# Kernel optimization log

Hardware: AMD Instinct MI355X
Metric: run time of the kernel (lower is better)

The kernel has to match this reference:

```python
import jax, jax.numpy as jnp
import numpy as np

FEATURE_SIZE = 1_000_000
FIELD_SIZE = 39
EMBED_SIZE = 32
HIDDEN = [400, 400]
BATCH = 16384


def setup_inputs() -> dict:
    key = jax.random.key(0)
    ks = jax.random.split(key, 10)
    p_emb = 1.0 / np.sqrt(FEATURE_SIZE + EMBED_SIZE)
    p_bias = 1.0 / np.sqrt(FEATURE_SIZE + 1)
    d_in = FIELD_SIZE * EMBED_SIZE
    p1 = 1.0 / np.sqrt(d_in + HIDDEN[0])
    p2 = 1.0 / np.sqrt(HIDDEN[0] + HIDDEN[1])
    d_cat = FIELD_SIZE + EMBED_SIZE + HIDDEN[-1]
    pf = 1.0 / np.sqrt(d_cat + 1)
    return {
        "feat_index": jax.random.randint(ks[0], (BATCH, FIELD_SIZE), 0, FEATURE_SIZE),
        "feat_value": jax.random.uniform(ks[1], (BATCH, FIELD_SIZE), dtype=jnp.float32),
        "feature_embedding": jax.random.uniform(ks[2], (FEATURE_SIZE, EMBED_SIZE), jnp.float32, -p_emb, p_emb),
        "feature_bias": jax.random.uniform(ks[3], (FEATURE_SIZE, 1), jnp.float32, -p_bias, p_bias),
        "W1": jax.random.uniform(ks[4], (HIDDEN[0], d_in), jnp.float32, -p1, p1),
        "b1": jnp.zeros((HIDDEN[0],), jnp.float32),
        "W2": jax.random.uniform(ks[5], (HIDDEN[1], HIDDEN[0]), jnp.float32, -p2, p2),
        "b2": jnp.zeros((HIDDEN[1],), jnp.float32),
        "final_W": jax.random.uniform(ks[6], (1, d_cat), jnp.float32, -pf, pf),
        "final_b": jnp.zeros((1,), jnp.float32),
    }


def reference(feat_index, feat_value, feature_embedding, feature_bias,
              W1, b1, W2, b2, final_W, final_b):
    B = feat_index.shape[0]
    fv = feat_value[:, :, None]                          # [B, F, 1]
    emb = feature_embedding[feat_index] * fv             # [B, F, E]

    # first-order FM term: [B, F]
    first_order = jnp.sum(feature_bias[feat_index] * fv, axis=-1)

    # second-order FM term: 0.5 * ((sum e)^2 - sum e^2), [B, E]
    sum_emb = jnp.sum(emb, axis=1)
    second_order = 0.5 * (sum_emb * sum_emb - jnp.sum(emb * emb, axis=1))

    # deep component
    deep_y = emb.reshape(B, FIELD_SIZE * EMBED_SIZE)
    deep_y = jax.nn.relu(deep_y @ W1.T + b1)
    deep_y = jax.nn.relu(deep_y @ W2.T + b2)

    concat_input = jnp.concatenate([first_order, second_order, deep_y], axis=1)
    output = concat_input @ final_W.T + final_b          # [B, 1]
    return (output, first_order, second_order, deep_y)
```

## Files before the change

kernel.cpp:

```cpp
#include <hip/hip_runtime.h>
#include <hip/hip_bf16.h>

#define BATCH 16384
#define FIELD 39
#define EMB 32
#define DIN (FIELD * EMB)
#define HID 400
#define DCAT (FIELD + EMB + HID)

typedef __attribute__((ext_vector_type(8))) short short8;
typedef __attribute__((ext_vector_type(4))) float float4v;

static __device__ __forceinline__ unsigned short f2bf(float f) {
    __hip_bfloat16 h = __float2bfloat16(f);
    return *(unsigned short*)&h;
}

__global__ __launch_bounds__(256) void gather_fm_kernel(
    const int* __restrict__ feat_index,
    const float* __restrict__ feat_value,
    const float* __restrict__ emb_table,
    const float* __restrict__ bias_table,
    unsigned short* __restrict__ emb_ws,
    float* __restrict__ first_order,
    float* __restrict__ second_order)
{
    __shared__ int   s_idx[FIELD];
    __shared__ float s_val[FIELD];
    __shared__ float s_emb[FIELD][EMB];

    const int r = blockIdx.x;
    const int t = threadIdx.x;

    if (t < FIELD) {
        int   idx = feat_index[r * FIELD + t];
        float val = feat_value[r * FIELD + t];
        s_idx[t] = idx;
        s_val[t] = val;
        first_order[r * FIELD + t] = bias_table[idx] * val;
    }
    __syncthreads();

    for (int e = t; e < DIN; e += 256) {
        const int f = e >> 5;
        const int j = e & 31;
        float v = emb_table[(size_t)s_idx[f] * EMB + j] * s_val[f];
        s_emb[f][j] = v;
        emb_ws[(size_t)r * DIN + e] = f2bf(v);
    }
    __syncthreads();

    if (t < EMB) {
        float s = 0.f, sq = 0.f;
        #pragma unroll
        for (int f = 0; f < FIELD; ++f) {
            float v = s_emb[f][t];
            s  += v;
            sq += v * v;
        }
        second_order[r * EMB + t] = 0.5f * (s * s - sq);
    }
}

__global__ __launch_bounds__(256) void cvt_weights(
    const float* __restrict__ W1, const float* __restrict__ W2,
    unsigned short* __restrict__ W1b, unsigned short* __restrict__ W2b,
    int n1, int n2)
{
    int i = blockIdx.x * 256 + threadIdx.x;
    if (i < n1)           W1b[i]      = f2bf(W1[i]);
    else if (i < n1 + n2) W2b[i - n1] = f2bf(W2[i - n1]);
}

template<bool OUT_BF16>
__global__ __launch_bounds__(256) void gemm_mfma_nt(
    const unsigned short* __restrict__ A,
    const unsigned short* __restrict__ Bw,
    const float* __restrict__ bias,
    void* __restrict__ Cp,
    int M, int N, int K)
{
    constexpr int BM = 128, BN = 128, BK = 32;
    constexpr int LDT = BK + 8;
    __shared__ __align__(16) unsigned short As[BM][LDT];
    __shared__ __align__(16) unsigned short Bs[BN][LDT];

    const int tid  = threadIdx.x;
    const int wave = tid >> 6;
    const int lane = tid & 63;
    const int quad = lane >> 4;
    const int l16  = lane & 15;
    const int wm = (wave & 1) * 64;
    const int wn = (wave >> 1) * 64;
    const int m0 = blockIdx.x * BM;
    const int n0 = blockIdx.y * BN;

    const int srow   = tid >> 2;
    const int schunk = (tid & 3) * 8;

    float4v acc[4][4];
    #pragma unroll
    for (int i = 0; i < 4; ++i)
        #pragma unroll
        for (int j = 0; j < 4; ++j)
            acc[i][j] = (float4v)(0.f);

    for (int k0 = 0; k0 < K; k0 += BK) {
        const bool kin = (k0 + schunk) < K;
        #pragma unroll
        for (int p = 0; p < 2; ++p) {
            const int row = p * 64 + srow;
            short8 av = (short8)0;
            if (kin)
                av = *(const short8*)(A + (size_t)(m0 + row) * K + k0 + schunk);
            *(short8*)(&As[row][schunk]) = av;
            short8 bv = (short8)0;
            if (kin && (n0 + row) < N)
                bv = *(const short8*)(Bw + (size_t)(n0 + row) * K + k0 + schunk);
            *(short8*)(&Bs[row][schunk]) = bv;
        }
        __syncthreads();

        short8 af[4], bf[4];
        #pragma unroll
        for (int i = 0; i < 4; ++i)
            af[i] = *(const short8*)(&As[wm + i * 16 + l16][quad * 8]);
        #pragma unroll
        for (int j = 0; j < 4; ++j)
            bf[j] = *(const short8*)(&Bs[wn + j * 16 + l16][quad * 8]);

        #pragma unroll
        for (int i = 0; i < 4; ++i)
            #pragma unroll
            for (int j = 0; j < 4; ++j)
                acc[i][j] = __builtin_amdgcn_mfma_f32_16x16x32_bf16(
                    af[i], bf[j], acc[i][j], 0, 0, 0);
        __syncthreads();
    }

    #pragma unroll
    for (int i = 0; i < 4; ++i) {
        const int rbase = m0 + wm + i * 16 + quad * 4;
        #pragma unroll
        for (int j = 0; j < 4; ++j) {
            const int col = n0 + wn + j * 16 + l16;
            if (col < N) {
                const float bv = bias[col];
                #pragma unroll
                for (int r2 = 0; r2 < 4; ++r2) {
                    float v = acc[i][j][r2] + bv;
                    v = v > 0.f ? v : 0.f;
                    if (OUT_BF16)
                        ((unsigned short*)Cp)[(size_t)(rbase + r2) * N + col] = f2bf(v);
                    else
                        ((float*)Cp)[(size_t)(rbase + r2) * N + col] = v;
                }
            }
        }
    }
}

__global__ __launch_bounds__(256) void final_kernel(
    const float* __restrict__ fo,
    const float* __restrict__ so,
    const float* __restrict__ dy,
    const float* __restrict__ fW,
    const float* __restrict__ fb,
    float* __restrict__ out)
{
    const int lane = threadIdx.x & 63;
    const int wave = threadIdx.x >> 6;
    const int r = blockIdx.x * 4 + wave;

    float s = 0.f;
    if (lane < FIELD)
        s += fo[(size_t)r * FIELD + lane] * fW[lane];
    if (lane < EMB)
        s += so[(size_t)r * EMB + lane] * fW[FIELD + lane];
    for (int e = lane; e < HID; e += 64)
        s += dy[(size_t)r * HID + e] * fW[FIELD + EMB + e];

    #pragma unroll
    for (int off = 32; off > 0; off >>= 1)
        s += __shfl_down(s, off, 64);

    if (lane == 0)
        out[r] = s + fb[0];
}

extern "C" void kernel_launch(void* const* d_in, const int* in_sizes, int n_in,
                              void* d_out, int out_size, void* d_ws, size_t ws_size,
                              hipStream_t stream)
{
    const int*   feat_index = (const int*)d_in[0];
    const float* feat_value = (const float*)d_in[1];
    const float* emb_table  = (const float*)d_in[2];
    const float* bias_table = (const float*)d_in[3];
    const float* W1         = (const float*)d_in[4];
    const float* b1         = (const float*)d_in[5];
    const float* W2         = (const float*)d_in[6];
    const float* b2         = (const float*)d_in[7];
    const float* fW         = (const float*)d_in[8];
    const float* fb         = (const float*)d_in[9];

    float* out = (float*)d_out;
    float* out0 = out;
    float* fo   = out + BATCH;
    float* so   = out + (size_t)BATCH * (1 + FIELD);
    float* dy   = out + (size_t)BATCH * (1 + FIELD + EMB);

    unsigned short* emb_ws = (unsigned short*)d_ws;
    unsigned short* h1     = emb_ws + (size_t)BATCH * DIN;
    unsigned short* W1b    = h1 + (size_t)BATCH * HID;
    unsigned short* W2b    = W1b + (size_t)HID * DIN;

    const int n1 = HID * DIN, n2 = HID * HID;
    cvt_weights<<<(n1 + n2 + 255) / 256, 256, 0, stream>>>(W1, W2, W1b, W2b, n1, n2);

    gather_fm_kernel<<<BATCH, 256, 0, stream>>>(
        feat_index, feat_value, emb_table, bias_table, emb_ws, fo, so);

    dim3 grid_g(BATCH / 128, (HID + 127) / 128);
    gemm_mfma_nt<true ><<<grid_g, 256, 0, stream>>>(emb_ws, W1b, b1, h1, BATCH, HID, DIN);
    gemm_mfma_nt<false><<<grid_g, 256, 0, stream>>>(h1,     W2b, b2, dy, BATCH, HID, HID);

    final_kernel<<<BATCH / 4, 256, 0, stream>>>(fo, so, dy, fW, fb, out0);
}
```

Measured before the change: 318.5 us.

## Use direct global-to-LDS loads with swizzle, padded weights, and wave-per-row gather

The GEMMs now stage tiles with global_load_lds into unpadded, XOR-swizzled LDS. The weights, biases and hidden buffer are zero-padded (N to 512, K2 to 416), so the tile loads need no bounds checks and K2 divides evenly by BK. The gather/FM kernel now handles one row per wave with float4 gathers and shuffle reductions instead of one row per block through shared memory. In exchange, the padding adds wasted MFMA work on the extra columns, and the h1 layout and its pad columns depend on the zeroed weights.

```diff
diff --git a/kernel.cpp b/kernel.cpp
--- a/kernel.cpp
+++ b/kernel.cpp
@@ -6,7 +6,8 @@
 #define EMB 32
 #define DIN (FIELD * EMB)
 #define HID 400
-#define DCAT (FIELD + EMB + HID)
+#define NPAD 512
+#define K2P 416
 
 typedef __attribute__((ext_vector_type(8))) short short8;
 typedef __attribute__((ext_vector_type(4))) float float4v;
@@ -25,65 +26,97 @@
     float* __restrict__ first_order,
     float* __restrict__ second_order)
 {
-    __shared__ int   s_idx[FIELD];
-    __shared__ float s_val[FIELD];
-    __shared__ float s_emb[FIELD][EMB];
-
-    const int r = blockIdx.x;
-    const int t = threadIdx.x;
-
-    if (t < FIELD) {
-        int   idx = feat_index[r * FIELD + t];
-        float val = feat_value[r * FIELD + t];
-        s_idx[t] = idx;
-        s_val[t] = val;
-        first_order[r * FIELD + t] = bias_table[idx] * val;
-    }
-    __syncthreads();
-
-    for (int e = t; e < DIN; e += 256) {
-        const int f = e >> 5;
-        const int j = e & 31;
-        float v = emb_table[(size_t)s_idx[f] * EMB + j] * s_val[f];
-        s_emb[f][j] = v;
-        emb_ws[(size_t)r * DIN + e] = f2bf(v);
-    }
-    __syncthreads();
-
-    if (t < EMB) {
-        float s = 0.f, sq = 0.f;
-        #pragma unroll
-        for (int f = 0; f < FIELD; ++f) {
-            float v = s_emb[f][t];
-            s  += v;
-            sq += v * v;
+    const int lane = threadIdx.x & 63;
+    const int wave = threadIdx.x >> 6;
+    const int r = blockIdx.x * 4 + wave;
+
+    int   idx0 = 0;
+    float val0 = 0.f;
+    if (lane < FIELD) {
+        idx0 = feat_index[r * FIELD + lane];
+        val0 = feat_value[r * FIELD + lane];
+        first_order[r * FIELD + lane] = bias_table[idx0] * val0;
+    }
+
+    const int fsub = lane >> 3;
+    const int j4   = (lane & 7) * 4;
+
+    float sx = 0.f, sy = 0.f, sz = 0.f, sw = 0.f;
+    float qx = 0.f, qy = 0.f, qz = 0.f, qw = 0.f;
+
+    #pragma unroll
+    for (int step = 0; step < 5; ++step) {
+        const int  f  = step * 8 + fsub;
+        const int  fi = __shfl(idx0, f, 64);
+        const float fv = __shfl(val0, f, 64);
+        const bool ok = (f < FIELD);
+        float4 e4 = make_float4(0.f, 0.f, 0.f, 0.f);
+        if (ok) {
+            float4 t = *(const float4*)(emb_table + (size_t)fi * EMB + j4);
+            e4.x = t.x * fv; e4.y = t.y * fv; e4.z = t.z * fv; e4.w = t.w * fv;
+            uint2 pk;
+            pk.x = (unsigned)f2bf(e4.x) | ((unsigned)f2bf(e4.y) << 16);
+            pk.y = (unsigned)f2bf(e4.z) | ((unsigned)f2bf(e4.w) << 16);
+            *(uint2*)(emb_ws + (size_t)r * DIN + step * 256 + lane * 4) = pk;
         }
-        second_order[r * EMB + t] = 0.5f * (s * s - sq);
+        sx += e4.x; sy += e4.y; sz += e4.z; sw += e4.w;
+        qx += e4.x * e4.x; qy += e4.y * e4.y; qz += e4.z * e4.z; qw += e4.w * e4.w;
+    }
+
+    #pragma unroll
+    for (int d = 8; d < 64; d <<= 1) {
+        sx += __shfl_xor(sx, d, 64); sy += __shfl_xor(sy, d, 64);
+        sz += __shfl_xor(sz, d, 64); sw += __shfl_xor(sw, d, 64);
+        qx += __shfl_xor(qx, d, 64); qy += __shfl_xor(qy, d, 64);
+        qz += __shfl_xor(qz, d, 64); qw += __shfl_xor(qw, d, 64);
+    }
+
+    if (lane < 8) {
+        float4 so4;
+        so4.x = 0.5f * (sx * sx - qx);
+        so4.y = 0.5f * (sy * sy - qy);
+        so4.z = 0.5f * (sz * sz - qz);
+        so4.w = 0.5f * (sw * sw - qw);
+        *(float4*)(second_order + (size_t)r * EMB + lane * 4) = so4;
     }
 }
 
 __global__ __launch_bounds__(256) void cvt_weights(
     const float* __restrict__ W1, const float* __restrict__ W2,
+    const float* __restrict__ b1, const float* __restrict__ b2,
     unsigned short* __restrict__ W1b, unsigned short* __restrict__ W2b,
-    int n1, int n2)
-{
+    float* __restrict__ b1p, float* __restrict__ b2p)
+{
+    const int n1p = NPAD * DIN;
+    const int n2p = NPAD * K2P;
     int i = blockIdx.x * 256 + threadIdx.x;
-    if (i < n1)           W1b[i]      = f2bf(W1[i]);
-    else if (i < n1 + n2) W2b[i - n1] = f2bf(W2[i - n1]);
+    if (i < n1p) {
+        int row = i / DIN, col = i - row * DIN;
+        W1b[i] = (row < HID) ? f2bf(W1[row * DIN + col]) : (unsigned short)0;
+    } else if (i < n1p + n2p) {
+        int j = i - n1p;
+        int row = j / K2P, col = j - row * K2P;
+        W2b[j] = (row < HID && col < HID) ? f2bf(W2[row * HID + col]) : (unsigned short)0;
+    } else if (i < n1p + n2p + NPAD) {
+        int k = i - n1p - n2p;
+        b1p[k] = (k < HID) ? b1[k] : 0.f;
+    } else if (i < n1p + n2p + 2 * NPAD) {
+        int k = i - n1p - n2p - NPAD;
+        b2p[k] = (k < HID) ? b2[k] : 0.f;
+    }
 }
 
 template<bool OUT_BF16>
-__global__ __launch_bounds__(256) void gemm_mfma_nt(
-    const unsigned short* __restrict__ A,
-    const unsigned short* __restrict__ Bw,
+__global__ __launch_bounds__(256) void gemm_mfma_gll(
+    const unsigned short* __restrict__ A, int lda,
+    const unsigned short* __restrict__ Bw, int ldb,
     const float* __restrict__ bias,
-    void* __restrict__ Cp,
-    int M, int N, int K)
+    void* __restrict__ Cp, int ldc, int stn,
+    int K)
 {
     constexpr int BM = 128, BN = 128, BK = 32;
-    constexpr int LDT = BK + 8;
-    __shared__ __align__(16) unsigned short As[BM][LDT];
-    __shared__ __align__(16) unsigned short Bs[BN][LDT];
+    __shared__ __align__(16) unsigned short As[BM][BK];
+    __shared__ __align__(16) unsigned short Bs[BN][BK];
 
     const int tid  = threadIdx.x;
     const int wave = tid >> 6;
@@ -95,8 +128,8 @@
     const int m0 = blockIdx.x * BM;
     const int n0 = blockIdx.y * BN;
 
-    const int srow   = tid >> 2;
-    const int schunk = (tid & 3) * 8;
+    const int sr   = lane >> 2;
+    const int slot = lane & 3;
 
     float4v acc[4][4];
     #pragma unroll
@@ -105,29 +138,34 @@
         for (int j = 0; j < 4; ++j)
             acc[i][j] = (float4v)(0.f);
 
+    const int fslot = (quad ^ (l16 & 3)) * 8;
+
     for (int k0 = 0; k0 < K; k0 += BK) {
-        const bool kin = (k0 + schunk) < K;
         #pragma unroll
         for (int p = 0; p < 2; ++p) {
-            const int row = p * 64 + srow;
-            short8 av = (short8)0;
-            if (kin)
-                av = *(const short8*)(A + (size_t)(m0 + row) * K + k0 + schunk);
-            *(short8*)(&As[row][schunk]) = av;
-            short8 bv = (short8)0;
-            if (kin && (n0 + row) < N)
-                bv = *(const short8*)(Bw + (size_t)(n0 + row) * K + k0 + schunk);
-            *(short8*)(&Bs[row][schunk]) = bv;
+            const int seg = wave * 2 + p;
+            const int r   = seg * 16 + sr;
+            const int c   = slot ^ (r & 3);
+            const unsigned short* gA = A + (size_t)(m0 + r) * lda + k0 + c * 8;
+            unsigned short* lA = &As[0][0] + seg * 512 + lane * 8;
+            __builtin_amdgcn_global_load_lds(
+                (const __attribute__((address_space(1))) unsigned int*)gA,
+                (__attribute__((address_space(3))) unsigned int*)lA, 16, 0, 0);
+            const unsigned short* gB = Bw + (size_t)(n0 + r) * ldb + k0 + c * 8;
+            unsigned short* lB = &Bs[0][0] + seg * 512 + lane * 8;
+            __builtin_amdgcn_global_load_lds(
+                (const __attribute__((address_space(1))) unsigned int*)gB,
+                (__attribute__((address_space(3))) unsigned int*)lB, 16, 0, 0);
         }
         __syncthreads();
 
         short8 af[4], bf[4];
         #pragma unroll
         for (int i = 0; i < 4; ++i)
-            af[i] = *(const short8*)(&As[wm + i * 16 + l16][quad * 8]);
+            af[i] = *(const short8*)(&As[wm + i * 16 + l16][fslot]);
         #pragma unroll
         for (int j = 0; j < 4; ++j)
-            bf[j] = *(const short8*)(&Bs[wn + j * 16 + l16][quad * 8]);
+            bf[j] = *(const short8*)(&Bs[wn + j * 16 + l16][fslot]);
 
         #pragma unroll
         for (int i = 0; i < 4; ++i)
@@ -144,16 +182,16 @@
         #pragma unroll
         for (int j = 0; j < 4; ++j) {
             const int col = n0 + wn + j * 16 + l16;
-            if (col < N) {
+            if (col < stn) {
                 const float bv = bias[col];
                 #pragma unroll
                 for (int r2 = 0; r2 < 4; ++r2) {
                     float v = acc[i][j][r2] + bv;
                     v = v > 0.f ? v : 0.f;
                     if (OUT_BF16)
-                        ((unsigned short*)Cp)[(size_t)(rbase + r2) * N + col] = f2bf(v);
+                        ((unsigned short*)Cp)[(size_t)(rbase + r2) * ldc + col] = f2bf(v);
                     else
-                        ((float*)Cp)[(size_t)(rbase + r2) * N + col] = v;
+                        ((float*)Cp)[(size_t)(rbase + r2) * ldc + col] = v;
                 }
             }
         }
@@ -211,18 +249,23 @@
 
     unsigned short* emb_ws = (unsigned short*)d_ws;
     unsigned short* h1     = emb_ws + (size_t)BATCH * DIN;
-    unsigned short* W1b    = h1 + (size_t)BATCH * HID;
-    unsigned short* W2b    = W1b + (size_t)HID * DIN;
-
-    const int n1 = HID * DIN, n2 = HID * HID;
-    cvt_weights<<<(n1 + n2 + 255) / 256, 256, 0, stream>>>(W1, W2, W1b, W2b, n1, n2);
-
-    gather_fm_kernel<<<BATCH, 256, 0, stream>>>(
+    unsigned short* W1b    = h1 + (size_t)BATCH * K2P;
+    unsigned short* W2b    = W1b + (size_t)NPAD * DIN;
+    float*          b1p    = (float*)(W2b + (size_t)NPAD * K2P);
+    float*          b2p    = b1p + NPAD;
+
+    const int ncvt = NPAD * DIN + NPAD * K2P + 2 * NPAD;
+    cvt_weights<<<(ncvt + 255) / 256, 256, 0, stream>>>(
+        W1, W2, b1, b2, W1b, W2b, b1p, b2p);
+
+    gather_fm_kernel<<<BATCH / 4, 256, 0, stream>>>(
         feat_index, feat_value, emb_table, bias_table, emb_ws, fo, so);
 
-    dim3 grid_g(BATCH / 128, (HID + 127) / 128);
-    gemm_mfma_nt<true ><<<grid_g, 256, 0, stream>>>(emb_ws, W1b, b1, h1, BATCH, HID, DIN);
-    gemm_mfma_nt<false><<<grid_g, 256, 0, stream>>>(h1,     W2b, b2, dy, BATCH, HID, HID);
+    dim3 grid_g(BATCH / 128, NPAD / 128);
+    gemm_mfma_gll<true ><<<grid_g, 256, 0, stream>>>(
+        emb_ws, DIN, W1b, DIN, b1p, h1, K2P, K2P, DIN);
+    gemm_mfma_gll<false><<<grid_g, 256, 0, stream>>>(
+        h1, K2P, W2b, K2P, b2p, dy, HID, HID, K2P);
 
     final_kernel<<<BATCH / 4, 256, 0, stream>>>(fo, so, dy, fW, fb, out0);
 }
```

Result: faster. 278.2 us (-12.7%).
